# Performance work log

Hardware: AMD Instinct MI355X
Metric: run time of the kernel (lower is better)

Reference implementation:

```python
import jax, jax.numpy as jnp
import numpy as np

N_Q = 16
N_K = 16
D_QK = 64
D_V = 64
# torch module default scale=1.0 saturates softmax at feature width 1024;
# we use the conventional sqrt(d) scale for well-conditioned numerics.
SCALE = 32.0  # sqrt(N_Q * D_QK)
DROPOUT_P = 0.0  # dropout is identity at p=0


def setup_inputs() -> dict:
    key = jax.random.key(0)
    kq, kk, kv = jax.random.split(key, 3)
    S = 8192
    return {
        "query": jax.random.normal(kq, (S, N_Q, D_QK), dtype=jnp.float32),
        "key": jax.random.normal(kk, (S, N_K, D_QK), dtype=jnp.float32),
        "value": jax.random.normal(kv, (S, N_K, D_V), dtype=jnp.float32),
    }


def reference(query, key, value):
    # Flatten trailing (head, dim) into one feature axis, as the torch view does.
    q = query.reshape(-1, N_Q * D_QK)            # [S_q, 1024]
    k = key.reshape(-1, N_K * D_QK)              # [S_k, 1024]
    v = value.reshape(-1, N_K * D_V)             # [S_k, 1024]
    scores = jnp.matmul(q, k.T) / SCALE          # [S_q, S_k]
    attn = jax.nn.softmax(scores, axis=-1)       # dropout_p=0 -> identity
    out = jnp.matmul(attn, v)                    # [S_q, 1024]
    return out.reshape(query.shape[:-1] + (-1,))  # [S_q, N_Q, D_V]
```

## Files before the change

### kernel.cpp

```cpp
#include <hip/hip_runtime.h>
#include <hip/hip_bf16.h>


typedef __bf16 bf16x8 __attribute__((ext_vector_type(8)));
typedef float f32x4 __attribute__((ext_vector_type(4)));
typedef const __attribute__((address_space(1))) unsigned int* as1p;
typedef __attribute__((address_space(3))) unsigned int* as3p;
typedef unsigned short u16;

__device__ __forceinline__ u16 f2bf(float x) {
  unsigned u = __float_as_uint(x);
  u += 0x7fffu + ((u >> 16) & 1u);
  return (u16)(u >> 16);
}
__device__ __forceinline__ float bf2f(u16 b) { return __uint_as_float(((unsigned)b) << 16); }
__device__ __forceinline__ unsigned pack2(float lo, float hi) {
  return (unsigned)f2bf(lo) | ((unsigned)f2bf(hi) << 16);
}

#define BAR()   do { __builtin_amdgcn_s_barrier(); __builtin_amdgcn_sched_barrier(0); } while (0)
#define LGKM0() do { asm volatile("s_waitcnt lgkmcnt(0)" ::: "memory"); __builtin_amdgcn_sched_barrier(0); } while (0)
#define VM(n)   do { asm volatile("s_waitcnt vmcnt(" #n ")" ::: "memory"); __builtin_amdgcn_sched_barrier(0); } while (0)

__global__ __launch_bounds__(256) void cvt_bf16(const float* __restrict__ in,
                                                unsigned short* __restrict__ out) {
  const size_t i = (size_t)blockIdx.x * 256 + threadIdx.x;
  const float4* p = (const float4*)in + i * 2;
  float4 a = p[0], b = p[1];
  uint4 o;
  o.x = pack2(a.x, a.y);
  o.y = pack2(a.z, a.w);
  o.z = pack2(b.x, b.y);
  o.w = pack2(b.z, b.w);
  ((uint4*)out)[i] = o;
}

__global__ __launch_bounds__(256) void transpose_bf16(const float* __restrict__ V,
                                                      unsigned short* __restrict__ VT) {
  __shared__ float t[64][65];
  const int rb = blockIdx.x * 64;
  const int cb = blockIdx.y * 64;
  const int tid = threadIdx.x;
#pragma unroll
  for (int it = 0; it < 4; ++it) {
    int r = it * 16 + (tid >> 4);
    int c = (tid & 15) * 4;
    float4 x = *(const float4*)(V + (size_t)(rb + r) * 1024 + cb + c);
    t[r][c] = x.x; t[r][c + 1] = x.y; t[r][c + 2] = x.z; t[r][c + 3] = x.w;
  }
  __syncthreads();
  const int j = tid & 63;
  const int c0 = (tid >> 6) * 16;
#pragma unroll
  for (int i = 0; i < 16; ++i) {
    int c = c0 + i;
    VT[(size_t)(cb + c) * 8192 + rb + j] = f2bf(t[j][c]);
  }
}

template <int BM, int OUTMODE>
__global__ __launch_bounds__(512, 2) void gemm8(const u16* __restrict__ A,
                                                const u16* __restrict__ B,
                                                void* __restrict__ Cv,
                                                const float* __restrict__ inv,
                                                float* __restrict__ partials,
                                                int K, int ldc, int ntn, float scale) {
  constexpr int MF = BM / 32;
  constexpr int MH = MF / 2;
  constexpr int LA = BM / 64;
  constexpr int NU = (LA + 4) / 2;
  constexpr int ABUF = BM * 128;
  constexpr int BBUF = 32768;
  constexpr int BUFSZ = ABUF + BBUF;
  static_assert(NU == 3 || NU == 4, "");
  __shared__ __align__(1024) char smem[2 * BUFSZ];

  const int tid = threadIdx.x;
  const int lane = tid & 63, wave = tid >> 6;
  const int wr = wave >> 2, wc = wave & 3;
  const int lan15 = lane & 15, g = lane >> 4, l7 = lane & 7;

  const int nwg = gridDim.x;
  const int wg = (blockIdx.x & 7) * (nwg >> 3) + (blockIdx.x >> 3);
  const int bm0 = (wg / ntn) * BM;
  const int bn0 = (wg % ntn) * 256;

  const int sr = tid >> 3;
  const int scb = ((tid & 7) ^ (sr & 7)) * 8;
  const u16* Ags = A + (size_t)(bm0 + sr) * K + scb;
  const u16* Bgs = B + (size_t)(bn0 + sr) * K + scb;

  const int sa0 = ((0 + g) ^ l7) * 16;
  const int sa1 = ((4 + g) ^ l7) * 16;
  const int abase = (wr * (BM / 2) + lan15) * 128;
  const int bbase = ABUF + (wc * 64 + lan15) * 128;

  f32x4 acc[MF][4];
#pragma unroll
  for (int m = 0; m < MF; ++m)
#pragma unroll
    for (int n = 0; n < 4; ++n) acc[m][n] = f32x4{0.f, 0.f, 0.f, 0.f};

  const int nt = K >> 6;
  const int niter = nt >> 1;

  auto ISSUE_UNIT = [&](int t, int u) {
    const int bb = (t & 1) * BUFSZ;
    const size_t ko = (size_t)t * 64;
    if (2 * u < LA) {
#pragma unroll
      for (int s = 0; s < 2; ++s) {
        const int j = 2 * u + s;
        __builtin_amdgcn_global_load_lds((as1p)(Ags + (size_t)j * 64 * K + ko),
                                         (as3p)(smem + bb + j * 8192 + tid * 16), 16, 0, 0);
      }
    } else {
#pragma unroll
      for (int s = 0; s < 2; ++s) {
        const int j = 2 * u - LA + s;
        __builtin_amdgcn_global_load_lds((as1p)(Bgs + (size_t)j * 64 * K + ko),
                                         (as3p)(smem + bb + ABUF + j * 8192 + tid * 16), 16, 0, 0);
      }
    }
  };

  bf16x8 a[MH][2], b[4][2];
  auto DS_A = [&](int bb, int mh) {
#pragma unroll
    for (int m = 0; m < MH; ++m) {
      a[m][0] = *(const bf16x8*)(smem + bb + abase + (mh * MH + m) * 2048 + sa0);
      a[m][1] = *(const bf16x8*)(smem + bb + abase + (mh * MH + m) * 2048 + sa1);
    }
  };
  auto DS_B = [&](int bb, int nh) {
#pragma unroll
    for (int n = 0; n < 2; ++n) {
      b[nh * 2 + n][0] = *(const bf16x8*)(smem + bb + bbase + (nh * 2 + n) * 2048 + sa0);
      b[nh * 2 + n][1] = *(const bf16x8*)(smem + bb + bbase + (nh * 2 + n) * 2048 + sa1);
    }
  };
  auto MMA = [&](int mh, int nh) {
    __builtin_amdgcn_s_setprio(1);
#pragma unroll
    for (int m = 0; m < MH; ++m)
#pragma unroll
      for (int n = 0; n < 2; ++n)
#pragma unroll
        for (int ks = 0; ks < 2; ++ks)
          acc[mh * MH + m][nh * 2 + n] = __builtin_amdgcn_mfma_f32_16x16x32_bf16(
              a[m][ks], b[nh * 2 + n][ks], acc[mh * MH + m][nh * 2 + n], 0, 0, 0);
    __builtin_amdgcn_s_setprio(0);
  };

#pragma unroll
  for (int u = 0; u < NU; ++u) ISSUE_UNIT(0, u);
  ISSUE_UNIT(1, 0);
  VM(2);
  BAR();

  for (int i = 0; i < niter; ++i) {
    const int t0 = 2 * i;
    const bool more = (i + 1 < niter);

    DS_A(0, 0); DS_B(0, 0);
    ISSUE_UNIT(t0 + 1, 1);
    BAR(); LGKM0(); MMA(0, 0); BAR();

    DS_B(0, 1);
    if constexpr (NU >= 3) ISSUE_UNIT(t0 + 1, 2);
    BAR(); LGKM0(); MMA(0, 1); BAR();

    DS_A(0, 1);
    if constexpr (NU >= 4) ISSUE_UNIT(t0 + 1, 3);
    BAR(); LGKM0(); MMA(1, 0); BAR();

    if (more) ISSUE_UNIT(t0 + 2, 0);
    BAR(); MMA(1, 1);
    if (more) { VM(2); } else { VM(0); }
    BAR();

    DS_A(BUFSZ, 0); DS_B(BUFSZ, 0);
    if (more) ISSUE_UNIT(t0 + 2, 1);
    BAR(); LGKM0(); MMA(0, 0); BAR();

    DS_B(BUFSZ, 1);
    if (more) { if constexpr (NU >= 3) ISSUE_UNIT(t0 + 2, 2); }
    BAR(); LGKM0(); MMA(0, 1); BAR();

    DS_A(BUFSZ, 1);
    if (more) { if constexpr (NU >= 4) ISSUE_UNIT(t0 + 2, 3); }
    BAR(); LGKM0(); MMA(1, 0); BAR();

    if (more) ISSUE_UNIT(t0 + 3, 0);
    BAR(); MMA(1, 1);
    if (more) { VM(2); } else { VM(0); }
    BAR();
  }

  const int c0 = bn0 + wc * 64 + lan15;
  if constexpr (OUTMODE == 0) {
    u16* C = (u16*)Cv;
    const int cb4 = (bn0 >> 8) * 4 + wc;
#pragma unroll
    for (int m = 0; m < MF; ++m)
#pragma unroll
      for (int r = 0; r < 4; ++r) {
        const int row = bm0 + wr * (BM / 2) + m * 16 + g * 4 + r;
        float part = 0.f;
#pragma unroll
        for (int n = 0; n < 4; ++n) {
          float v = __expf(acc[m][n][r] * scale);
          C[(size_t)row * ldc + c0 + n * 16] = f2bf(v);
          part += v;
        }
        part += __shfl_xor(part, 1, 64);
        part += __shfl_xor(part, 2, 64);
        part += __shfl_xor(part, 4, 64);
        part += __shfl_xor(part, 8, 64);
        if (lan15 == 0) partials[(size_t)row * 128 + cb4] = part;
      }
  } else {
    float* C = (float*)Cv;
#pragma unroll
    for (int m = 0; m < MF; ++m)
#pragma unroll
      for (int r = 0; r < 4; ++r) {
        const int row = bm0 + wr * (BM / 2) + m * 16 + g * 4 + r;
        const float iv = inv ? inv[row] : 1.0f;
#pragma unroll
        for (int n = 0; n < 4; ++n)
          C[(size_t)row * ldc + c0 + n * 16] = acc[m][n][r] * iv;
      }
  }
}

__global__ __launch_bounds__(256) void rowinv(const float* __restrict__ partials,
                                              float* __restrict__ inv) {
  const int row = blockIdx.x * 256 + threadIdx.x;
  const float4* p = (const float4*)(partials + (size_t)row * 128);
  float s = 0.f;
#pragma unroll
  for (int j = 0; j < 32; ++j) {
    float4 v = p[j];
    s += (v.x + v.y) + (v.z + v.w);
  }
  inv[row] = 1.0f / s;
}

__global__ __launch_bounds__(256) void normalize_inplace(u16* __restrict__ E) {
  __shared__ float red[4];
  u16* row = E + (size_t)blockIdx.x * 8192;
  const int tid = threadIdx.x;
  float f[32];
  float s = 0.f;
#pragma unroll
  for (int c = 0; c < 4; ++c) {
    uint4 v = *((const uint4*)row + c * 256 + tid);
    unsigned u[4] = {v.x, v.y, v.z, v.w};
#pragma unroll
    for (int q = 0; q < 4; ++q) {
      f[c * 8 + q * 2] = bf2f((u16)(u[q] & 0xffffu));
      f[c * 8 + q * 2 + 1] = bf2f((u16)(u[q] >> 16));
      s += f[c * 8 + q * 2] + f[c * 8 + q * 2 + 1];
    }
  }
#pragma unroll
  for (int off = 32; off; off >>= 1) s += __shfl_xor(s, off, 64);
  if ((tid & 63) == 0) red[tid >> 6] = s;
  __syncthreads();
  const float iv = 1.0f / ((red[0] + red[1]) + (red[2] + red[3]));
#pragma unroll
  for (int c = 0; c < 4; ++c) {
    uint4 o;
    o.x = pack2(f[c * 8 + 0] * iv, f[c * 8 + 1] * iv);
    o.y = pack2(f[c * 8 + 2] * iv, f[c * 8 + 3] * iv);
    o.z = pack2(f[c * 8 + 4] * iv, f[c * 8 + 5] * iv);
    o.w = pack2(f[c * 8 + 6] * iv, f[c * 8 + 7] * iv);
    *((uint4*)row + c * 256 + tid) = o;
  }
}

extern "C" void kernel_launch(void* const* d_in, const int* in_sizes, int n_in,
                              void* d_out, int out_size, void* d_ws, size_t ws_size,
                              hipStream_t stream) {
  const float* Q = (const float*)d_in[0];
  const float* K = (const float*)d_in[1];
  const float* V = (const float*)d_in[2];

  char* ws = (char*)d_ws;
  u16* S = (u16*)ws;
  u16* VT = (u16*)(ws + (size_t)134217728);
  float* partials = (float*)(ws + (size_t)134217728 + 16777216);
  float* inv = (float*)(ws + (size_t)134217728 + 16777216 + 4194304);
  const bool haveInv =
      ws_size >= (size_t)134217728 + 16777216 + 4194304 + 32768;

  u16* Qb = (u16*)d_out;
  u16* Kb = Qb + 8388608;

  cvt_bf16<<<4096, 256, 0, stream>>>(Q, Qb);
  cvt_bf16<<<4096, 256, 0, stream>>>(K, Kb);
  transpose_bf16<<<dim3(128, 16), 256, 0, stream>>>(V, VT);

  gemm8<256, 0><<<1024, 512, 0, stream>>>(
      Qb, Kb, S, nullptr, haveInv ? partials : (float*)(ws + 134217728 + 16777216),
      1024, 8192, 32, 1.0f / 32.0f);

  if (haveInv) {
    rowinv<<<32, 256, 0, stream>>>(partials, inv);
    gemm8<128, 1><<<256, 512, 0, stream>>>(
        S, VT, d_out, inv, nullptr, 8192, 1024, 4, 1.0f);
  } else {
    normalize_inplace<<<8192, 256, 0, stream>>>(S);
    gemm8<128, 1><<<256, 512, 0, stream>>>(
        S, VT, d_out, nullptr, nullptr, 8192, 1024, 4, 1.0f);
  }
}
```

Measured before the change: 310.4 us.

## Relax LDS waits in GEMM main loop and remap tile order

Drops the explicit full lgkmcnt(0) waits before each MFMA phase and lets the compiler insert finer-grained waits for the LDS-read results instead. One wait is kept after the third MMA of each half-iteration so buffer reuse stays safe. The barrier macro now uses a plain memory clobber rather than sched_barrier, which gives the scheduler more freedom to interleave ds_reads with MFMAs. It also replaces the generic wg/ntn tile decode with hardcoded mappings: QK^T groups 8 column tiles per row band for L2 reuse, and PV iterates M fastest. The risks are relying on compiler-inserted waitcnts across the barrier sequence and hardcoded grid shapes.

```diff
diff --git a/kernel.cpp b/kernel.cpp
--- a/kernel.cpp
+++ b/kernel.cpp
@@ -18,7 +18,7 @@
   return (unsigned)f2bf(lo) | ((unsigned)f2bf(hi) << 16);
 }
 
-#define BAR()   do { __builtin_amdgcn_s_barrier(); __builtin_amdgcn_sched_barrier(0); } while (0)
+#define BAR()   do { __builtin_amdgcn_s_barrier(); asm volatile("" ::: "memory"); } while (0)
 #define LGKM0() do { asm volatile("s_waitcnt lgkmcnt(0)" ::: "memory"); __builtin_amdgcn_sched_barrier(0); } while (0)
 #define VM(n)   do { asm volatile("s_waitcnt vmcnt(" #n ")" ::: "memory"); __builtin_amdgcn_sched_barrier(0); } while (0)
 
@@ -58,13 +58,13 @@
   }
 }
 
-template <int BM, int OUTMODE>
+template <int BM, int OUTMODE, int DEC>
 __global__ __launch_bounds__(512, 2) void gemm8(const u16* __restrict__ A,
                                                 const u16* __restrict__ B,
                                                 void* __restrict__ Cv,
                                                 const float* __restrict__ inv,
                                                 float* __restrict__ partials,
-                                                int K, int ldc, int ntn, float scale) {
+                                                int K, int ldc, float scale) {
   constexpr int MF = BM / 32;
   constexpr int MH = MF / 2;
   constexpr int LA = BM / 64;
@@ -82,8 +82,16 @@
 
   const int nwg = gridDim.x;
   const int wg = (blockIdx.x & 7) * (nwg >> 3) + (blockIdx.x >> 3);
-  const int bm0 = (wg / ntn) * BM;
-  const int bn0 = (wg % ntn) * 256;
+
+  int bm0, bn0;
+  if constexpr (DEC == 0) {
+    const int r = wg & 255;
+    bm0 = (r >> 3) * 256;
+    bn0 = (((wg >> 8) << 3) | (r & 7)) * 256;
+  } else {
+    bm0 = (wg & 63) * BM;
+    bn0 = (wg >> 6) * 256;
+  }
 
   const int sr = tid >> 3;
   const int scb = ((tid & 7) ^ (sr & 7)) * 8;
@@ -164,15 +172,15 @@
 
     DS_A(0, 0); DS_B(0, 0);
     ISSUE_UNIT(t0 + 1, 1);
-    BAR(); LGKM0(); MMA(0, 0); BAR();
+    BAR(); MMA(0, 0); BAR();
 
     DS_B(0, 1);
     if constexpr (NU >= 3) ISSUE_UNIT(t0 + 1, 2);
-    BAR(); LGKM0(); MMA(0, 1); BAR();
+    BAR(); MMA(0, 1); BAR();
 
     DS_A(0, 1);
     if constexpr (NU >= 4) ISSUE_UNIT(t0 + 1, 3);
-    BAR(); LGKM0(); MMA(1, 0); BAR();
+    BAR(); MMA(1, 0); LGKM0(); BAR();
 
     if (more) ISSUE_UNIT(t0 + 2, 0);
     BAR(); MMA(1, 1);
@@ -181,15 +189,15 @@
 
     DS_A(BUFSZ, 0); DS_B(BUFSZ, 0);
     if (more) ISSUE_UNIT(t0 + 2, 1);
-    BAR(); LGKM0(); MMA(0, 0); BAR();
+    BAR(); MMA(0, 0); BAR();
 
     DS_B(BUFSZ, 1);
     if (more) { if constexpr (NU >= 3) ISSUE_UNIT(t0 + 2, 2); }
-    BAR(); LGKM0(); MMA(0, 1); BAR();
+    BAR(); MMA(0, 1); BAR();
 
     DS_A(BUFSZ, 1);
     if (more) { if constexpr (NU >= 4) ISSUE_UNIT(t0 + 2, 3); }
-    BAR(); LGKM0(); MMA(1, 0); BAR();
+    BAR(); MMA(1, 0); LGKM0(); BAR();
 
     if (more) ISSUE_UNIT(t0 + 3, 0);
     BAR(); MMA(1, 1);
@@ -302,17 +310,17 @@
   cvt_bf16<<<4096, 256, 0, stream>>>(K, Kb);
   transpose_bf16<<<dim3(128, 16), 256, 0, stream>>>(V, VT);
 
-  gemm8<256, 0><<<1024, 512, 0, stream>>>(
+  gemm8<256, 0, 0><<<1024, 512, 0, stream>>>(
       Qb, Kb, S, nullptr, haveInv ? partials : (float*)(ws + 134217728 + 16777216),
-      1024, 8192, 32, 1.0f / 32.0f);
+      1024, 8192, 1.0f / 32.0f);
 
   if (haveInv) {
     rowinv<<<32, 256, 0, stream>>>(partials, inv);
-    gemm8<128, 1><<<256, 512, 0, stream>>>(
-        S, VT, d_out, inv, nullptr, 8192, 1024, 4, 1.0f);
+    gemm8<128, 1, 1><<<256, 512, 0, stream>>>(
+        S, VT, d_out, inv, nullptr, 8192, 1024, 1.0f);
   } else {
     normalize_inplace<<<8192, 256, 0, stream>>>(S);
-    gemm8<128, 1><<<256, 512, 0, stream>>>(
-        S, VT, d_out, nullptr, nullptr, 8192, 1024, 4, 1.0f);
-  }
-}
+    gemm8<128, 1, 1><<<256, 512, 0, stream>>>(
+        S, VT, d_out, nullptr, nullptr, 8192, 1024, 1.0f);
+  }
+}
```

Result: no change. 305.6 us (-1.5%).
